# Optimization experiments

Hardware: AMD Instinct MI355X
Metric: run time of the kernel (lower is better)

Reference implementation:

```python
import jax, jax.numpy as jnp
import numpy as np
from jax import lax

BATCH, SEQ_LEN, HIDDEN, CLASSES = 512, 256, 1024, 128

def _xavier(key, shape):
    fan_out, fan_in = shape
    std = float(np.sqrt(2.0 / (fan_in + fan_out)))
    return jax.random.normal(key, shape, dtype=jnp.float32) * std

def setup_inputs() -> dict:
    key = jax.random.key(0)
    k_x, k_hx, k_hh, k_ph = jax.random.split(key, 4)
    return {
        "x": jax.random.normal(k_x, (BATCH, SEQ_LEN), dtype=jnp.float32),
        "W_hx": _xavier(k_hx, (HIDDEN, 1)),
        "W_hh": _xavier(k_hh, (HIDDEN, HIDDEN)),
        "b_h": jnp.zeros((HIDDEN,), dtype=jnp.float32),
        "W_ph": _xavier(k_ph, (CLASSES, HIDDEN)),
        "b_p": jnp.zeros((CLASSES,), dtype=jnp.float32),
    }

def reference(x, W_hx, W_hh, b_h, W_ph, b_p):
    # x: [B, T] (input_dim == 1 per timestep, as in the torch module)
    B = x.shape[0]
    H = W_hh.shape[0]
    h0 = jnp.zeros((B, H), dtype=x.dtype)

    def step(h, xt):
        # xt: [B]; xt[:, None] @ W_hx.T -> [B, H]
        h_new = jnp.tanh(xt[:, None] @ W_hx.T + h @ W_hh.T + b_h)
        return h_new, None

    h_last, _ = lax.scan(step, h0, x.T)  # scan over time: x.T is [T, B]
    # Output head applied to final hidden state (loop's last p in torch code)
    return h_last @ W_ph.T + b_p  # [B, num_classes]
```

## Files before the change

kernel.cpp:

```cpp
#include <hip/hip_runtime.h>
#include <stdint.h>


#define BATCH 512
#define SEQ   256
#define HID   1024
#define CLS   128

#define GB 16
#define GJ 16
#define BT 32
#define JT 64
#define KC 256
#define WSTR 1028
#define SSTR 260
#define HSTR 68
#define SMEM_BYTES ((JT * WSTR + BT * SSTR) * 2)
#define HBUF_HALVES (BATCH * HID)

typedef __attribute__((ext_vector_type(8))) short  bf16x8;
typedef __attribute__((ext_vector_type(4))) short  s16x4;
typedef __attribute__((ext_vector_type(4))) float  f32x4;
typedef __attribute__((ext_vector_type(4))) int    i32x4;
typedef __attribute__((ext_vector_type(2))) unsigned int u32x2;

__device__ __forceinline__ unsigned short f2bf(float f) {
  unsigned int u = __float_as_uint(f);
  u = (u + 0x7FFFu + ((u >> 16) & 1u)) >> 16;
  return (unsigned short)u;
}
__device__ __forceinline__ float b2f(short h) {
  return __uint_as_float(((unsigned int)(unsigned short)h) << 16);
}

__device__ __forceinline__ void store_flag(int* p, int v) {
  asm volatile("global_store_dword %0, %1, off sc0 sc1" :: "v"(p), "v"(v) : "memory");
}
__device__ __forceinline__ int load_flag(const int* p) {
  int v;
  asm volatile("global_load_dword %0, %1, off sc0 sc1\n\t"
               "s_waitcnt vmcnt(0)" : "=v"(v) : "v"(p) : "memory");
  return v;
}
__device__ __forceinline__ void store16(void* p, i32x4 v) {
  asm volatile("global_store_dwordx4 %0, %1, off sc0 sc1" :: "v"(p), "v"(v) : "memory");
}
__device__ __forceinline__ void waitcnt0() {
  asm volatile("s_waitcnt vmcnt(0)" ::: "memory");
}
__device__ __forceinline__ void barrier_lgkm() {
  asm volatile("s_waitcnt lgkmcnt(0)\n\ts_barrier" ::: "memory");
}
__device__ __forceinline__ void issue4(const void* p, i32x4& a, i32x4& b, i32x4& c, i32x4& d) {
  asm volatile(
    "global_load_dwordx4 %0, %4, off sc0 sc1\n\t"
    "global_load_dwordx4 %1, %4, off offset:128 sc0 sc1\n\t"
    "global_load_dwordx4 %2, %4, off offset:256 sc0 sc1\n\t"
    "global_load_dwordx4 %3, %4, off offset:384 sc0 sc1"
    : "=&v"(a), "=&v"(b), "=&v"(c), "=&v"(d)
    : "v"(p) : "memory");
}
#define DEF_WAIT(NAME, N) \
__device__ __forceinline__ void NAME(i32x4& a, i32x4& b, i32x4& c, i32x4& d) { \
  asm volatile("s_waitcnt vmcnt(" #N ")" : "+v"(a), "+v"(b), "+v"(c), "+v"(d) :: "memory"); \
}
DEF_WAIT(wait_vm12, 12)
DEF_WAIT(wait_vm8, 8)
DEF_WAIT(wait_vm4, 4)
DEF_WAIT(wait_vm0, 0)

__device__ __forceinline__ void wr16(short* p, i32x4 v) {
  u32x2 lo, hi;
  lo.x = (unsigned)v.x; lo.y = (unsigned)v.y;
  hi.x = (unsigned)v.z; hi.y = (unsigned)v.w;
  *(u32x2*)p = lo;
  *(u32x2*)(p + 4) = hi;
}
__device__ __forceinline__ bf16x8 ld8(const short* p) {
  union { bf16x8 v8; s16x4 h[2]; } u;
  u.h[0] = *(const s16x4*)p;
  u.h[1] = *(const s16x4*)(p + 4);
  return u.v8;
}
__device__ __forceinline__ float tanh_fast(float z) {
  float e = __expf(2.f * z);
  return 1.f - 2.f / (e + 1.f);
}

__device__ __forceinline__ void mfma_chunk(const short* sW, const short* sS,
                                           int wv, int l15, int quad, int c,
                                           f32x4& acc0, f32x4& acc1) {
  const short* Brow  = sW + (wv * 16 + l15) * WSTR + c * KC + quad * 8;
  const short* Arow0 = sS + l15 * SSTR + quad * 8;
  const short* Arow1 = Arow0 + 16 * SSTR;
#pragma unroll
  for (int ks = 0; ks < 8; ++ks) {
    bf16x8 bfr = ld8(Brow  + ks * 32);
    bf16x8 a0  = ld8(Arow0 + ks * 32);
    bf16x8 a1  = ld8(Arow1 + ks * 32);
    acc0 = __builtin_amdgcn_mfma_f32_16x16x32_bf16(a0, bfr, acc0, 0, 0, 0);
    acc1 = __builtin_amdgcn_mfma_f32_16x16x32_bf16(a1, bfr, acc1, 0, 0, 0);
  }
}

__global__ void __launch_bounds__(256, 1)
rnn_persistent(const float* __restrict__ x, const float* __restrict__ Whx,
               const float* __restrict__ Whh, const float* __restrict__ bh,
               const float* __restrict__ Wph, const float* __restrict__ bp,
               float* __restrict__ out, unsigned short* hbuf, int* flags)
{
  extern __shared__ short smem[];
  short* sW = smem;
  short* sS = smem + JT * WSTR;

  const int tid  = threadIdx.x;
  const int bg   = blockIdx.x & 15;
  const int jg   = blockIdx.x >> 4;
  const int lane = tid & 63;
  const int wv   = tid >> 6;
  const int l15  = lane & 15;
  const int quad = lane >> 4;

  {
    const int jr = tid >> 2;
    const int kq = tid & 3;
    const float* src = Whh + (jg * JT + jr) * HID + kq * 256;
    short* dst = sW + jr * WSTR + kq * 256;
#pragma unroll 4
    for (int i = 0; i < 64; ++i) {
      float4 f = *(const float4*)(src + i * 4);
      s16x4 h4;
      h4.x = (short)f2bf(f.x); h4.y = (short)f2bf(f.y);
      h4.z = (short)f2bf(f.z); h4.w = (short)f2bf(f.w);
      *(s16x4*)(dst + i * 4) = h4;
    }
  }

  const int j = jg * JT + wv * 16 + l15;
  const float whx = Whx[j];
  const float bhv = bh[j];
  const int grow0 = bg * BT + quad * 4;

  const int sr  = tid >> 3;
  const int seg = tid & 7;

  int* myflags = flags + bg * 64;

  for (int t = 0; t < SEQ; ++t) {
    const unsigned short* hin = hbuf + ((t + 1) & 1) * HBUF_HALVES;
    unsigned short*      hout = hbuf + (t & 1) * HBUF_HALVES;

    f32x4 acc0 = {0.f, 0.f, 0.f, 0.f};
    f32x4 acc1 = {0.f, 0.f, 0.f, 0.f};

    float xv0[4], xv1[4];
    {
      const float* xp = x + grow0 * SEQ + t;
#pragma unroll
      for (int rg = 0; rg < 4; ++rg) {
        xv0[rg] = xp[rg * SEQ];
        xv1[rg] = xp[(16 + rg) * SEQ];
      }
    }

    if (t > 0) {
      if (tid < GJ) {
        while (load_flag(myflags + tid) < t) {}
      }
      __syncthreads();

      const char* lbase = (const char*)(hin + (bg * BT + sr) * HID) + seg * 16;
      short* sdst = sS + sr * SSTR + seg * 8;

      i32x4 a0, a1, a2, a3, b0, b1, b2, b3, c0, c1, c2, c3, d0, d1, d2, d3;
      issue4(lbase,        a0, a1, a2, a3);
      issue4(lbase + 512,  b0, b1, b2, b3);
      issue4(lbase + 1024, c0, c1, c2, c3);
      issue4(lbase + 1536, d0, d1, d2, d3);

      wait_vm12(a0, a1, a2, a3);
      wr16(sdst, a0); wr16(sdst + 64, a1); wr16(sdst + 128, a2); wr16(sdst + 192, a3);
      barrier_lgkm();
      mfma_chunk(sW, sS, wv, l15, quad, 0, acc0, acc1);

      barrier_lgkm();
      wait_vm8(b0, b1, b2, b3);
      wr16(sdst, b0); wr16(sdst + 64, b1); wr16(sdst + 128, b2); wr16(sdst + 192, b3);
      barrier_lgkm();
      mfma_chunk(sW, sS, wv, l15, quad, 1, acc0, acc1);

      barrier_lgkm();
      wait_vm4(c0, c1, c2, c3);
      wr16(sdst, c0); wr16(sdst + 64, c1); wr16(sdst + 128, c2); wr16(sdst + 192, c3);
      barrier_lgkm();
      mfma_chunk(sW, sS, wv, l15, quad, 2, acc0, acc1);

      barrier_lgkm();
      wait_vm0(d0, d1, d2, d3);
      wr16(sdst, d0); wr16(sdst + 64, d1); wr16(sdst + 128, d2); wr16(sdst + 192, d3);
      barrier_lgkm();
      mfma_chunk(sW, sS, wv, l15, quad, 3, acc0, acc1);
    }

    barrier_lgkm();
    {
      short* hS = sS;
#pragma unroll
      for (int rg = 0; rg < 4; ++rg) {
        float z0 = acc0[rg] + xv0[rg] * whx + bhv;
        hS[(quad * 4 + rg) * HSTR + wv * 16 + l15] = (short)f2bf(tanh_fast(z0));
        float z1 = acc1[rg] + xv1[rg] * whx + bhv;
        hS[(16 + quad * 4 + rg) * HSTR + wv * 16 + l15] = (short)f2bf(tanh_fast(z1));
      }
    }
    barrier_lgkm();
    {
      const short* hsrc = sS + sr * HSTR + seg * 8;
      u32x2 lo = *(const u32x2*)(hsrc);
      u32x2 hi = *(const u32x2*)(hsrc + 4);
      i32x4 sv; sv.x = (int)lo.x; sv.y = (int)lo.y; sv.z = (int)hi.x; sv.w = (int)hi.y;
      unsigned short* dst = hout + (bg * BT + sr) * HID + jg * JT + seg * 8;
      store16(dst, sv);
    }
    waitcnt0();
    barrier_lgkm();
    if (tid == 0) store_flag(myflags + jg, t + 1);
  }

  if (tid < GJ) {
    while (load_flag(myflags + tid) < SEQ) {}
  }
  __syncthreads();

  const unsigned short* hlast = hbuf + ((SEQ - 1) & 1) * HBUF_HALVES;
  const int cc = tid & 7;
  const int cg = jg * 8 + cc;
  const int hr = tid >> 3;
  float acc = 0.f;
  const char* lbase = (const char*)(hlast + (bg * BT + sr) * HID) + seg * 16;
  short* sdst = sS + sr * SSTR + seg * 8;
  for (int c = 0; c < 4; ++c) {
    __syncthreads();
    i32x4 p0, p1, p2, p3;
    issue4(lbase + c * 512, p0, p1, p2, p3);
    waitcnt0();
    wr16(sdst, p0); wr16(sdst + 64, p1); wr16(sdst + 128, p2); wr16(sdst + 192, p3);
    __syncthreads();
    const float* wp = Wph + cg * HID + c * KC;
    const short* hs = sS + hr * SSTR;
#pragma unroll 8
    for (int k4 = 0; k4 < 64; ++k4) {
      float4 w  = *(const float4*)(wp + k4 * 4);
      s16x4 hv  = *(const s16x4*)(hs + k4 * 4);
      acc += b2f(hv.x) * w.x + b2f(hv.y) * w.y + b2f(hv.z) * w.z + b2f(hv.w) * w.w;
    }
  }
  out[(bg * BT + hr) * CLS + cg] = acc + bp[cg];
}

extern "C" void kernel_launch(void* const* d_in, const int* in_sizes, int n_in,
                              void* d_out, int out_size, void* d_ws, size_t ws_size,
                              hipStream_t stream) {
  const float* x   = (const float*)d_in[0];
  const float* Whx = (const float*)d_in[1];
  const float* Whh = (const float*)d_in[2];
  const float* bh  = (const float*)d_in[3];
  const float* Wph = (const float*)d_in[4];
  const float* bp  = (const float*)d_in[5];
  float* out = (float*)d_out;

  unsigned short* hbuf = (unsigned short*)d_ws;
  int* flags = (int*)((char*)d_ws + (size_t)2 * HBUF_HALVES * 2);

  hipFuncSetAttribute(reinterpret_cast<const void*>(rnn_persistent),
                      hipFuncAttributeMaxDynamicSharedMemorySize, SMEM_BYTES);

  rnn_persistent<<<dim3(GB * GJ), dim3(256), SMEM_BYTES, stream>>>(
      x, Whx, Whh, bh, Wph, bp, out, hbuf, flags);
}
```

Before: 1.062 ms.

## Replace flag barriers with poisoned-sentinel ring buffer for hidden-state handoff

```diff
diff --git a/kernel.cpp b/kernel.cpp
--- a/kernel.cpp
+++ b/kernel.cpp
@@ -15,7 +15,9 @@
 #define WSTR 1028
 #define SSTR 260
 #define HSTR 68
-#define SMEM_BYTES ((JT * WSTR + BT * SSTR) * 2)
+#define NBUF 6
+#define XBSTR 33
+#define SMEM_BYTES ((JT * WSTR + BT * SSTR) * 2 + BT * XBSTR * 4)
 #define HBUF_HALVES (BATCH * HID)
 
 typedef __attribute__((ext_vector_type(8))) short  bf16x8;
@@ -33,15 +35,6 @@
   return __uint_as_float(((unsigned int)(unsigned short)h) << 16);
 }
 
-__device__ __forceinline__ void store_flag(int* p, int v) {
-  asm volatile("global_store_dword %0, %1, off sc0 sc1" :: "v"(p), "v"(v) : "memory");
-}
-__device__ __forceinline__ int load_flag(const int* p) {
-  int v;
-  asm volatile("global_load_dword %0, %1, off sc0 sc1\n\t"
-               "s_waitcnt vmcnt(0)" : "=v"(v) : "v"(p) : "memory");
-  return v;
-}
 __device__ __forceinline__ void store16(void* p, i32x4 v) {
   asm volatile("global_store_dwordx4 %0, %1, off sc0 sc1" :: "v"(p), "v"(v) : "memory");
 }
@@ -85,6 +78,20 @@
 __device__ __forceinline__ float tanh_fast(float z) {
   float e = __expf(2.f * z);
   return 1.f - 2.f / (e + 1.f);
+}
+
+__device__ __forceinline__ bool poisoned4(const i32x4& a, const i32x4& b,
+                                          const i32x4& c, const i32x4& d) {
+  return ((a.x & 0xFFFF) == 0xFFFF) | ((b.x & 0xFFFF) == 0xFFFF) |
+         ((c.x & 0xFFFF) == 0xFFFF) | ((d.x & 0xFFFF) == 0xFFFF);
+}
+__device__ __forceinline__ void retry4(const void* p, i32x4& a, i32x4& b,
+                                       i32x4& c, i32x4& d) {
+  do {
+    asm volatile("s_sleep 1" ::: "memory");
+    issue4(p, a, b, c, d);
+    waitcnt0();
+  } while (poisoned4(a, b, c, d));
 }
 
 __device__ __forceinline__ void mfma_chunk(const short* sW, const short* sS,
@@ -107,11 +114,12 @@
 rnn_persistent(const float* __restrict__ x, const float* __restrict__ Whx,
                const float* __restrict__ Whh, const float* __restrict__ bh,
                const float* __restrict__ Wph, const float* __restrict__ bp,
-               float* __restrict__ out, unsigned short* hbuf, int* flags)
+               float* __restrict__ out, unsigned short* hbuf)
 {
   extern __shared__ short smem[];
   short* sW = smem;
   short* sS = smem + JT * WSTR;
+  float* xb = (float*)(smem + JT * WSTR + BT * SSTR);
 
   const int tid  = threadIdx.x;
   const int bg   = blockIdx.x & 15;
@@ -139,36 +147,47 @@
   const int j = jg * JT + wv * 16 + l15;
   const float whx = Whx[j];
   const float bhv = bh[j];
-  const int grow0 = bg * BT + quad * 4;
 
   const int sr  = tid >> 3;
   const int seg = tid & 7;
 
-  int* myflags = flags + bg * 64;
+  int bw = 0, br = NBUF - 1, bz = 3;
 
   for (int t = 0; t < SEQ; ++t) {
-    const unsigned short* hin = hbuf + ((t + 1) & 1) * HBUF_HALVES;
-    unsigned short*      hout = hbuf + (t & 1) * HBUF_HALVES;
+    const unsigned short* hin = hbuf + br * HBUF_HALVES;
+    unsigned short*      hout = hbuf + bw * HBUF_HALVES;
+
+    if ((t & 31) == 0) {
+      barrier_lgkm();
+      const int xr = tid >> 3;
+      const int xc = (tid & 7) * 4;
+      float4 xt = *(const float4*)(x + (bg * BT + xr) * SEQ + t + xc);
+      xb[xr * XBSTR + xc + 0] = xt.x;
+      xb[xr * XBSTR + xc + 1] = xt.y;
+      xb[xr * XBSTR + xc + 2] = xt.z;
+      xb[xr * XBSTR + xc + 3] = xt.w;
+      __syncthreads();
+    }
+    float xv0[4], xv1[4];
+    {
+      const int tc = t & 31;
+#pragma unroll
+      for (int rg = 0; rg < 4; ++rg) {
+        xv0[rg] = xb[(quad * 4 + rg) * XBSTR + tc];
+        xv1[rg] = xb[(16 + quad * 4 + rg) * XBSTR + tc];
+      }
+    }
 
     f32x4 acc0 = {0.f, 0.f, 0.f, 0.f};
     f32x4 acc1 = {0.f, 0.f, 0.f, 0.f};
 
-    float xv0[4], xv1[4];
     {
-      const float* xp = x + grow0 * SEQ + t;
-#pragma unroll
-      for (int rg = 0; rg < 4; ++rg) {
-        xv0[rg] = xp[rg * SEQ];
-        xv1[rg] = xp[(16 + rg) * SEQ];
-      }
+      unsigned short* pb = hbuf + bz * HBUF_HALVES;
+      i32x4 pv; pv.x = -1; pv.y = -1; pv.z = -1; pv.w = -1;
+      store16(pb + (bg * BT + sr) * HID + jg * JT + seg * 8, pv);
     }
 
     if (t > 0) {
-      if (tid < GJ) {
-        while (load_flag(myflags + tid) < t) {}
-      }
-      __syncthreads();
-
       const char* lbase = (const char*)(hin + (bg * BT + sr) * HID) + seg * 16;
       short* sdst = sS + sr * SSTR + seg * 8;
 
@@ -179,24 +198,45 @@
       issue4(lbase + 1536, d0, d1, d2, d3);
 
       wait_vm12(a0, a1, a2, a3);
+      if (__builtin_expect(poisoned4(a0, a1, a2, a3), 0)) {
+        waitcnt0();
+        do {
+          asm volatile("s_sleep 1" ::: "memory");
+          issue4(lbase,        a0, a1, a2, a3);
+          issue4(lbase + 512,  b0, b1, b2, b3);
+          issue4(lbase + 1024, c0, c1, c2, c3);
+          issue4(lbase + 1536, d0, d1, d2, d3);
+          waitcnt0();
+        } while (poisoned4(a0, a1, a2, a3) || poisoned4(b0, b1, b2, b3) ||
+                 poisoned4(c0, c1, c2, c3) || poisoned4(d0, d1, d2, d3));
+      }
       wr16(sdst, a0); wr16(sdst + 64, a1); wr16(sdst + 128, a2); wr16(sdst + 192, a3);
       barrier_lgkm();
       mfma_chunk(sW, sS, wv, l15, quad, 0, acc0, acc1);
 
       barrier_lgkm();
       wait_vm8(b0, b1, b2, b3);
+      if (__builtin_expect(poisoned4(b0, b1, b2, b3), 0)) {
+        waitcnt0(); retry4(lbase + 512, b0, b1, b2, b3);
+      }
       wr16(sdst, b0); wr16(sdst + 64, b1); wr16(sdst + 128, b2); wr16(sdst + 192, b3);
       barrier_lgkm();
       mfma_chunk(sW, sS, wv, l15, quad, 1, acc0, acc1);
 
       barrier_lgkm();
       wait_vm4(c0, c1, c2, c3);
+      if (__builtin_expect(poisoned4(c0, c1, c2, c3), 0)) {
+        waitcnt0(); retry4(lbase + 1024, c0, c1, c2, c3);
+      }
       wr16(sdst, c0); wr16(sdst + 64, c1); wr16(sdst + 128, c2); wr16(sdst + 192, c3);
       barrier_lgkm();
       mfma_chunk(sW, sS, wv, l15, quad, 2, acc0, acc1);
 
       barrier_lgkm();
       wait_vm0(d0, d1, d2, d3);
+      if (__builtin_expect(poisoned4(d0, d1, d2, d3), 0)) {
+        retry4(lbase + 1536, d0, d1, d2, d3);
+      }
       wr16(sdst, d0); wr16(sdst + 64, d1); wr16(sdst + 128, d2); wr16(sdst + 192, d3);
       barrier_lgkm();
       mfma_chunk(sW, sS, wv, l15, quad, 3, acc0, acc1);
@@ -219,20 +259,18 @@
       u32x2 lo = *(const u32x2*)(hsrc);
       u32x2 hi = *(const u32x2*)(hsrc + 4);
       i32x4 sv; sv.x = (int)lo.x; sv.y = (int)lo.y; sv.z = (int)hi.x; sv.w = (int)hi.y;
+      if (t == 0) waitcnt0();
       unsigned short* dst = hout + (bg * BT + sr) * HID + jg * JT + seg * 8;
       store16(dst, sv);
     }
-    waitcnt0();
     barrier_lgkm();
-    if (tid == 0) store_flag(myflags + jg, t + 1);
+
+    bw = (bw + 1 == NBUF) ? 0 : bw + 1;
+    br = (br + 1 == NBUF) ? 0 : br + 1;
+    bz = (bz + 1 == NBUF) ? 0 : bz + 1;
   }
 
-  if (tid < GJ) {
-    while (load_flag(myflags + tid) < SEQ) {}
-  }
-  __syncthreads();
-
-  const unsigned short* hlast = hbuf + ((SEQ - 1) & 1) * HBUF_HALVES;
+  const unsigned short* hlast = hbuf + ((SEQ - 1) % NBUF) * HBUF_HALVES;
   const int cc = tid & 7;
   const int cg = jg * 8 + cc;
   const int hr = tid >> 3;
@@ -244,6 +282,7 @@
     i32x4 p0, p1, p2, p3;
     issue4(lbase + c * 512, p0, p1, p2, p3);
     waitcnt0();
+    if (poisoned4(p0, p1, p2, p3)) retry4(lbase + c * 512, p0, p1, p2, p3);
     wr16(sdst, p0); wr16(sdst + 64, p1); wr16(sdst + 128, p2); wr16(sdst + 192, p3);
     __syncthreads();
     const float* wp = Wph + cg * HID + c * KC;
@@ -270,11 +309,12 @@
   float* out = (float*)d_out;
 
   unsigned short* hbuf = (unsigned short*)d_ws;
-  int* flags = (int*)((char*)d_ws + (size_t)2 * HBUF_HALVES * 2);
+
+  hipMemsetAsync(d_ws, 0xFF, (size_t)3 * HBUF_HALVES * 2, stream);
 
   hipFuncSetAttribute(reinterpret_cast<const void*>(rnn_persistent),
                       hipFuncAttributeMaxDynamicSharedMemorySize, SMEM_BYTES);
 
   rnn_persistent<<<dim3(GB * GJ), dim3(256), SMEM_BYTES, stream>>>(
-      x, Whx, Whh, bh, Wph, bp, out, hbuf, flags);
-}
+      x, Whx, Whh, bh, Wph, bp, out, hbuf);
+}
```

Result: slower. 1.228 ms (+15.7%).

## Use 2x2 MFMA register tiling with split-K across waves and LDS reduction

Applied to the files above, without the earlier changes.

```diff
diff --git a/kernel.cpp b/kernel.cpp
--- a/kernel.cpp
+++ b/kernel.cpp
@@ -17,6 +17,7 @@
 #define HSTR 68
 #define SMEM_BYTES ((JT * WSTR + BT * SSTR) * 2)
 #define HBUF_HALVES (BATCH * HID)
+#define RED_OFF 2176
 
 typedef __attribute__((ext_vector_type(8))) short  bf16x8;
 typedef __attribute__((ext_vector_type(4))) short  s16x4;
@@ -87,19 +88,24 @@
   return 1.f - 2.f / (e + 1.f);
 }
 
-__device__ __forceinline__ void mfma_chunk(const short* sW, const short* sS,
-                                           int wv, int l15, int quad, int c,
-                                           f32x4& acc0, f32x4& acc1) {
-  const short* Brow  = sW + (wv * 16 + l15) * WSTR + c * KC + quad * 8;
-  const short* Arow0 = sS + l15 * SSTR + quad * 8;
-  const short* Arow1 = Arow0 + 16 * SSTR;
+__device__ __forceinline__ void mfma_chunk22(const short* sW, const short* sS,
+                                             int cp, int kh, int l15, int quad, int c,
+                                             f32x4& a00, f32x4& a01,
+                                             f32x4& a10, f32x4& a11) {
+  const short* B0  = sW + (cp * 32 + l15) * WSTR + c * KC + kh * 128 + quad * 8;
+  const short* B1  = B0 + 16 * WSTR;
+  const short* Ar0 = sS + l15 * SSTR + kh * 128 + quad * 8;
+  const short* Ar1 = Ar0 + 16 * SSTR;
 #pragma unroll
-  for (int ks = 0; ks < 8; ++ks) {
-    bf16x8 bfr = ld8(Brow  + ks * 32);
-    bf16x8 a0  = ld8(Arow0 + ks * 32);
-    bf16x8 a1  = ld8(Arow1 + ks * 32);
-    acc0 = __builtin_amdgcn_mfma_f32_16x16x32_bf16(a0, bfr, acc0, 0, 0, 0);
-    acc1 = __builtin_amdgcn_mfma_f32_16x16x32_bf16(a1, bfr, acc1, 0, 0, 0);
+  for (int i = 0; i < 4; ++i) {
+    bf16x8 b0 = ld8(B0  + i * 32);
+    bf16x8 b1 = ld8(B1  + i * 32);
+    bf16x8 a0 = ld8(Ar0 + i * 32);
+    bf16x8 a1 = ld8(Ar1 + i * 32);
+    a00 = __builtin_amdgcn_mfma_f32_16x16x32_bf16(a0, b0, a00, 0, 0, 0);
+    a10 = __builtin_amdgcn_mfma_f32_16x16x32_bf16(a1, b0, a10, 0, 0, 0);
+    a01 = __builtin_amdgcn_mfma_f32_16x16x32_bf16(a0, b1, a01, 0, 0, 0);
+    a11 = __builtin_amdgcn_mfma_f32_16x16x32_bf16(a1, b1, a11, 0, 0, 0);
   }
 }
 
@@ -120,6 +126,8 @@
   const int wv   = tid >> 6;
   const int l15  = lane & 15;
   const int quad = lane >> 4;
+  const int cp   = wv & 1;
+  const int kh   = wv >> 1;
 
   {
     const int jr = tid >> 2;
@@ -136,9 +144,10 @@
     }
   }
 
-  const int j = jg * JT + wv * 16 + l15;
-  const float whx = Whx[j];
-  const float bhv = bh[j];
+  const int j0 = jg * JT + cp * 32 + l15;
+  const int j1 = j0 + 16;
+  const float whx0 = Whx[j0], whx1 = Whx[j1];
+  const float bhv0 = bh[j0],  bhv1 = bh[j1];
   const int grow0 = bg * BT + quad * 4;
 
   const int sr  = tid >> 3;
@@ -150,8 +159,10 @@
     const unsigned short* hin = hbuf + ((t + 1) & 1) * HBUF_HALVES;
     unsigned short*      hout = hbuf + (t & 1) * HBUF_HALVES;
 
-    f32x4 acc0 = {0.f, 0.f, 0.f, 0.f};
-    f32x4 acc1 = {0.f, 0.f, 0.f, 0.f};
+    f32x4 acc00 = {0.f, 0.f, 0.f, 0.f};
+    f32x4 acc01 = {0.f, 0.f, 0.f, 0.f};
+    f32x4 acc10 = {0.f, 0.f, 0.f, 0.f};
+    f32x4 acc11 = {0.f, 0.f, 0.f, 0.f};
 
     float xv0[4], xv1[4];
     {
@@ -181,36 +192,53 @@
       wait_vm12(a0, a1, a2, a3);
       wr16(sdst, a0); wr16(sdst + 64, a1); wr16(sdst + 128, a2); wr16(sdst + 192, a3);
       barrier_lgkm();
-      mfma_chunk(sW, sS, wv, l15, quad, 0, acc0, acc1);
+      mfma_chunk22(sW, sS, cp, kh, l15, quad, 0, acc00, acc01, acc10, acc11);
 
       barrier_lgkm();
       wait_vm8(b0, b1, b2, b3);
       wr16(sdst, b0); wr16(sdst + 64, b1); wr16(sdst + 128, b2); wr16(sdst + 192, b3);
       barrier_lgkm();
-      mfma_chunk(sW, sS, wv, l15, quad, 1, acc0, acc1);
+      mfma_chunk22(sW, sS, cp, kh, l15, quad, 1, acc00, acc01, acc10, acc11);
 
       barrier_lgkm();
       wait_vm4(c0, c1, c2, c3);
       wr16(sdst, c0); wr16(sdst + 64, c1); wr16(sdst + 128, c2); wr16(sdst + 192, c3);
       barrier_lgkm();
-      mfma_chunk(sW, sS, wv, l15, quad, 2, acc0, acc1);
+      mfma_chunk22(sW, sS, cp, kh, l15, quad, 2, acc00, acc01, acc10, acc11);
 
       barrier_lgkm();
       wait_vm0(d0, d1, d2, d3);
       wr16(sdst, d0); wr16(sdst + 64, d1); wr16(sdst + 128, d2); wr16(sdst + 192, d3);
       barrier_lgkm();
-      mfma_chunk(sW, sS, wv, l15, quad, 3, acc0, acc1);
+      mfma_chunk22(sW, sS, cp, kh, l15, quad, 3, acc00, acc01, acc10, acc11);
     }
 
     barrier_lgkm();
     {
+      float* red = (float*)(sS + RED_OFF);
+      f32x4 w0 = kh ? acc00 : acc10;
+      f32x4 w1 = kh ? acc01 : acc11;
+      *(f32x4*)(red + tid * 8)     = w0;
+      *(f32x4*)(red + tid * 8 + 4) = w1;
+    }
+    barrier_lgkm();
+    {
+      const float* red = (const float*)(sS + RED_OFF);
+      const int ptid = tid ^ 128;
+      f32x4 r0 = *(const f32x4*)(red + ptid * 8);
+      f32x4 r1 = *(const f32x4*)(red + ptid * 8 + 4);
+      f32x4 f0 = (kh ? acc10 : acc00) + r0;
+      f32x4 f1 = (kh ? acc11 : acc01) + r1;
+
       short* hS = sS;
+      const int rbase = kh * 16 + quad * 4;
 #pragma unroll
       for (int rg = 0; rg < 4; ++rg) {
-        float z0 = acc0[rg] + xv0[rg] * whx + bhv;
-        hS[(quad * 4 + rg) * HSTR + wv * 16 + l15] = (short)f2bf(tanh_fast(z0));
-        float z1 = acc1[rg] + xv1[rg] * whx + bhv;
-        hS[(16 + quad * 4 + rg) * HSTR + wv * 16 + l15] = (short)f2bf(tanh_fast(z1));
+        float xr = kh ? xv1[rg] : xv0[rg];
+        float z0 = f0[rg] + xr * whx0 + bhv0;
+        hS[(rbase + rg) * HSTR + cp * 32 + l15] = (short)f2bf(tanh_fast(z0));
+        float z1 = f1[rg] + xr * whx1 + bhv1;
+        hS[(rbase + rg) * HSTR + cp * 32 + 16 + l15] = (short)f2bf(tanh_fast(z1));
       }
     }
     barrier_lgkm();
```

Result: faster. 1.028 ms (-3.1%).

## Load recurrent hidden-state fragments directly from global memory, skipping LDS staging

Applied to the files above, without the earlier changes.

```diff
diff --git a/kernel.cpp b/kernel.cpp
--- a/kernel.cpp
+++ b/kernel.cpp
@@ -48,6 +48,9 @@
 __device__ __forceinline__ void waitcnt0() {
   asm volatile("s_waitcnt vmcnt(0)" ::: "memory");
 }
+__device__ __forceinline__ void l1_inv_wait() {
+  asm volatile("buffer_inv sc0\n\ts_waitcnt vmcnt(0)" ::: "memory");
+}
 __device__ __forceinline__ void barrier_lgkm() {
   asm volatile("s_waitcnt lgkmcnt(0)\n\ts_barrier" ::: "memory");
 }
@@ -60,14 +63,6 @@
     : "=&v"(a), "=&v"(b), "=&v"(c), "=&v"(d)
     : "v"(p) : "memory");
 }
-#define DEF_WAIT(NAME, N) \
-__device__ __forceinline__ void NAME(i32x4& a, i32x4& b, i32x4& c, i32x4& d) { \
-  asm volatile("s_waitcnt vmcnt(" #N ")" : "+v"(a), "+v"(b), "+v"(c), "+v"(d) :: "memory"); \
-}
-DEF_WAIT(wait_vm12, 12)
-DEF_WAIT(wait_vm8, 8)
-DEF_WAIT(wait_vm4, 4)
-DEF_WAIT(wait_vm0, 0)
 
 __device__ __forceinline__ void wr16(short* p, i32x4 v) {
   u32x2 lo, hi;
@@ -82,25 +77,14 @@
   u.h[1] = *(const s16x4*)(p + 4);
   return u.v8;
 }
+__device__ __forceinline__ bf16x8 ldg8(const short* p) {
+  union { bf16x8 v8; i32x4 i4; } u;
+  u.i4 = *(const i32x4*)p;
+  return u.v8;
+}
 __device__ __forceinline__ float tanh_fast(float z) {
   float e = __expf(2.f * z);
   return 1.f - 2.f / (e + 1.f);
-}
-
-__device__ __forceinline__ void mfma_chunk(const short* sW, const short* sS,
-                                           int wv, int l15, int quad, int c,
-                                           f32x4& acc0, f32x4& acc1) {
-  const short* Brow  = sW + (wv * 16 + l15) * WSTR + c * KC + quad * 8;
-  const short* Arow0 = sS + l15 * SSTR + quad * 8;
-  const short* Arow1 = Arow0 + 16 * SSTR;
-#pragma unroll
-  for (int ks = 0; ks < 8; ++ks) {
-    bf16x8 bfr = ld8(Brow  + ks * 32);
-    bf16x8 a0  = ld8(Arow0 + ks * 32);
-    bf16x8 a1  = ld8(Arow1 + ks * 32);
-    acc0 = __builtin_amdgcn_mfma_f32_16x16x32_bf16(a0, bfr, acc0, 0, 0, 0);
-    acc1 = __builtin_amdgcn_mfma_f32_16x16x32_bf16(a1, bfr, acc1, 0, 0, 0);
-  }
 }
 
 __global__ void __launch_bounds__(256, 1)
@@ -144,6 +128,8 @@
   const int sr  = tid >> 3;
   const int seg = tid & 7;
 
+  const short* pB = sW + (wv * 16 + l15) * WSTR + quad * 8;
+
   int* myflags = flags + bg * 64;
 
   for (int t = 0; t < SEQ; ++t) {
@@ -167,42 +153,22 @@
       if (tid < GJ) {
         while (load_flag(myflags + tid) < t) {}
       }
+      if (tid == 0) l1_inv_wait();
       __syncthreads();
 
-      const char* lbase = (const char*)(hin + (bg * BT + sr) * HID) + seg * 16;
-      short* sdst = sS + sr * SSTR + seg * 8;
-
-      i32x4 a0, a1, a2, a3, b0, b1, b2, b3, c0, c1, c2, c3, d0, d1, d2, d3;
-      issue4(lbase,        a0, a1, a2, a3);
-      issue4(lbase + 512,  b0, b1, b2, b3);
-      issue4(lbase + 1024, c0, c1, c2, c3);
-      issue4(lbase + 1536, d0, d1, d2, d3);
-
-      wait_vm12(a0, a1, a2, a3);
-      wr16(sdst, a0); wr16(sdst + 64, a1); wr16(sdst + 128, a2); wr16(sdst + 192, a3);
-      barrier_lgkm();
-      mfma_chunk(sW, sS, wv, l15, quad, 0, acc0, acc1);
-
-      barrier_lgkm();
-      wait_vm8(b0, b1, b2, b3);
-      wr16(sdst, b0); wr16(sdst + 64, b1); wr16(sdst + 128, b2); wr16(sdst + 192, b3);
-      barrier_lgkm();
-      mfma_chunk(sW, sS, wv, l15, quad, 1, acc0, acc1);
-
-      barrier_lgkm();
-      wait_vm4(c0, c1, c2, c3);
-      wr16(sdst, c0); wr16(sdst + 64, c1); wr16(sdst + 128, c2); wr16(sdst + 192, c3);
-      barrier_lgkm();
-      mfma_chunk(sW, sS, wv, l15, quad, 2, acc0, acc1);
-
-      barrier_lgkm();
-      wait_vm0(d0, d1, d2, d3);
-      wr16(sdst, d0); wr16(sdst + 64, d1); wr16(sdst + 128, d2); wr16(sdst + 192, d3);
-      barrier_lgkm();
-      mfma_chunk(sW, sS, wv, l15, quad, 3, acc0, acc1);
-    }
-
-    barrier_lgkm();
+      const short* pA0 = (const short*)hin + (bg * BT + l15) * HID + quad * 8;
+      const short* pA1 = pA0 + 16 * HID;
+
+#pragma unroll
+      for (int ks = 0; ks < 32; ++ks) {
+        bf16x8 a0 = ldg8(pA0 + ks * 32);
+        bf16x8 a1 = ldg8(pA1 + ks * 32);
+        bf16x8 b  = ld8(pB + ks * 32);
+        acc0 = __builtin_amdgcn_mfma_f32_16x16x32_bf16(a0, b, acc0, 0, 0, 0);
+        acc1 = __builtin_amdgcn_mfma_f32_16x16x32_bf16(a1, b, acc1, 0, 0, 0);
+      }
+    }
+
     {
       short* hS = sS;
 #pragma unroll
@@ -272,6 +238,8 @@
   unsigned short* hbuf = (unsigned short*)d_ws;
   int* flags = (int*)((char*)d_ws + (size_t)2 * HBUF_HALVES * 2);
 
+  hipMemsetAsync(flags, 0, GB * 64 * sizeof(int), stream);
+
   hipFuncSetAttribute(reinterpret_cast<const void*>(rnn_persistent),
                       hipFuncAttributeMaxDynamicSharedMemorySize, SMEM_BYTES);
 
```

Measured after the change: 2.315 ms. 2.18x slower.
